# Kernel optimization log

Measured on AMD Instinct MI355X. Metric: run time of the kernel, lower is better.

Reference implementation:

```python
import jax, jax.numpy as jnp
import numpy as np


def _sig_gram(X, Y, n):
    """Signature-kernel gram matrix via the Goursat PDE recurrence.
    X: (A, M, D), Y: (B, N, D). Returns (A, B) of k(x_a, y_b).
    Recurrence: K[i+1,j+1] = K[i+1,j] + K[i,j+1] + K[i,j]*(inc_ij - 1).
    """
    f = 2 ** n
    # dyadic refinement: increments scaled by 1/2^n, each repeated 2^n times
    dX = jnp.repeat((X[:, 1:] - X[:, :-1]) / f, f, axis=1)  # (A, Mg-1, D)
    dY = jnp.repeat((Y[:, 1:] - Y[:, :-1]) / f, f, axis=1)  # (B, Ng-1, D)
    inc = jnp.einsum('aid,bjd->abij', dX, dY)               # (A, B, Mg-1, Ng-1)
    A, B, _, Ng1 = inc.shape
    ones_col = jnp.ones((A, B, 1), inc.dtype)

    def row_step(K_prev, inc_row):
        # K_prev: row i of the PDE grid, shape (A,B,Ng1+1); inc_row: (A,B,Ng1)
        diag = K_prev[..., :-1] * (inc_row - 1.0)  # K[i,j]*inc - K[i,j]
        up = K_prev[..., 1:]                        # K[i,j+1]

        def col_step(k_left, uv):
            u, d = uv
            k = k_left + u + d
            return k, k

        _, krow = jax.lax.scan(
            col_step,
            jnp.ones((A, B), inc.dtype),
            (jnp.moveaxis(up, -1, 0), jnp.moveaxis(diag, -1, 0)),
        )
        K_new = jnp.concatenate([ones_col, jnp.moveaxis(krow, 0, -1)], axis=-1)
        return K_new, None

    K0 = jnp.ones((A, B, Ng1 + 1), inc.dtype)  # boundary row K[0,:] = 1
    K_last, _ = jax.lax.scan(row_step, K0, jnp.moveaxis(inc, 2, 0))
    return K_last[..., -1]  # K[-1,-1] for every pair


def setup_inputs() -> dict:
    key = jax.random.key(0)
    kx, ky = jax.random.split(key)
    SCALE = 0.05  # keep kernel values in fp32 range (exponential growth)
    X = jax.random.normal(kx, (64, 128, 16), dtype=jnp.float32) * SCALE
    Y = jax.random.normal(ky, (64, 128, 16), dtype=jnp.float32) * SCALE
    return {"X": X, "Y": Y, "n": 0}


def reference(X, Y, n):
    k_xx = _sig_gram(X, X, n)
    k_yy = _sig_gram(Y, Y, n)
    k_xy = _sig_gram(X, Y, n)
    return jnp.mean(k_xx) + jnp.mean(k_yy) - 2.0 * jnp.mean(k_xy)
```

## Files before the change

kernel.cpp:

```cpp
#include <hip/hip_runtime.h>


typedef float f2 __attribute__((ext_vector_type(2)));

#define XY_BLOCKS 1024
#define TRI_BLOCKS 544
#define NBLOCKS (XY_BLOCKS + 2 * TRI_BLOCKS)

template <int C, int RM, int BM, bool BC>
__device__ __forceinline__ float dpp0(float x) {
    return __builtin_bit_cast(float, __builtin_amdgcn_update_dpp(
        0, __builtin_bit_cast(int, x), C, RM, BM, BC));
}

__device__ __forceinline__ float wave_scan_incl(float v) {
    v += dpp0<0x111, 0xf, 0xf, true>(v);
    v += dpp0<0x112, 0xf, 0xf, true>(v);
    v += dpp0<0x114, 0xf, 0xf, true>(v);
    v += dpp0<0x118, 0xf, 0xf, true>(v);
    v += dpp0<0x142, 0xa, 0xf, false>(v);
    v += dpp0<0x143, 0xc, 0xf, false>(v);
    return v;
}

__device__ __forceinline__ float wave_shr1(float x, float oldv) {
    return __builtin_bit_cast(float, __builtin_amdgcn_update_dpp(
        __builtin_bit_cast(int, oldv), __builtin_bit_cast(int, x),
        0x138, 0xf, 0xf, false));
}

__device__ __forceinline__ void load_xrow(f2* x, const float4* Ar, int r) {
#pragma unroll
    for (int q = 0; q < 4; ++q) {
        float4 v = Ar[4 * r + q];
        x[2*q].x   = v.x; x[2*q].y   = v.y;
        x[2*q+1].x = v.z; x[2*q+1].y = v.w;
    }
}

__device__ __forceinline__ void pde_row(
    const f2* xr, const f2* ya, const f2* yb,
    float& qpA, float& qpB, float& g_lo, float& g_hi, int lane)
{
    f2 s0 = 0.0f, s1 = 0.0f, t0 = 0.0f, t1 = 0.0f;
#pragma unroll
    for (int d = 0; d < 8; d += 2) {
        s0 = __builtin_elementwise_fma(xr[d],   ya[d],   s0);
        s1 = __builtin_elementwise_fma(xr[d+1], ya[d+1], s1);
        t0 = __builtin_elementwise_fma(xr[d],   yb[d],   t0);
        t1 = __builtin_elementwise_fma(xr[d+1], yb[d+1], t1);
    }
    const f2 sA = s0 + s1, sB = t0 + t1;
    const float hA = sA.x + sA.y, hB = sB.x + sB.y;
    const float i0 = hA - qpA;  qpA = hA + 1.0f;
    const float i1 = hB - qpB;  qpB = hB + 1.0f;
    const float gl = wave_shr1(g_hi, 1.0f);
    const float c0 = fmaf(gl, i0, g_lo);
    const float c1 = (lane == 63) ? 0.0f : fmaf(g_lo, i1, g_hi);
    const float S = wave_scan_incl(c0 + c1);
    g_lo = (S - c1) + 1.0f;
    g_hi = S + 1.0f;
}

__global__ __launch_bounds__(256) void sig_pde4(
    const float* __restrict__ X, const float* __restrict__ Y,
    float* __restrict__ outp)
{
    __shared__ float red[4];
    const int wv = threadIdx.x >> 6, lane = threadIdx.x & 63;
    const int B = blockIdx.x;

    int g, a, b;
    if (B < XY_BLOCKS) {
        g = 2; a = B >> 4; b = ((B & 15) << 2) + wv;
    } else {
        int t = B - XY_BLOCKS; g = 0;
        if (t >= TRI_BLOCKS) { t -= TRI_BLOCKS; g = 1; }
        int aa = 0;
        for (;;) { int nb = (67 - aa) >> 2; if (t < nb) break; t -= nb; ++aa; }
        a = aa; b = aa + (t << 2) + wv;
    }
    float weight = (g == 2) ? (-2.0f / 4096.0f)
                            : ((a == b ? 1.0f : 2.0f) / 4096.0f);
    if (g < 2 && b > 63) { b = 63; weight = 0.0f; }

    const float* P = (g == 1) ? Y : X;
    const float* Q = (g == 0) ? X : Y;

    f2 ya[8], yb[8];
    {
        const float* Qb = Q + b * 2048;
        const int j0 = lane << 1;
        const int j2 = (j0 + 2 <= 127) ? j0 + 2 : 127;
        const float4* A4 = (const float4*)(Qb + j0 * 16);
        const float4* B4 = (const float4*)(Qb + (j0 + 1) * 16);
        const float4* C4 = (const float4*)(Qb + j2 * 16);
#pragma unroll
        for (int q = 0; q < 4; ++q) {
            float4 ra = A4[q], rb = B4[q], rc = C4[q];
            ya[2*q].x   = rb.x - ra.x;  ya[2*q].y   = rb.y - ra.y;
            ya[2*q+1].x = rb.z - ra.z;  ya[2*q+1].y = rb.w - ra.w;
            yb[2*q].x   = rc.x - rb.x;  yb[2*q].y   = rc.y - rb.y;
            yb[2*q+1].x = rc.z - rb.z;  yb[2*q+1].y = rc.w - rb.w;
        }
    }

    const int abase = __builtin_amdgcn_readfirstlane(a * 2048);
    const float4* Ar = (const float4*)(P + abase);

    f2 xa[8], xb[8];
    float qpA, qpB;

    load_xrow(xa, Ar, 0);
    {
        f2 s0 = 0.0f, s1 = 0.0f, t0 = 0.0f, t1 = 0.0f;
#pragma unroll
        for (int d = 0; d < 8; d += 2) {
            s0 = __builtin_elementwise_fma(xa[d],   ya[d],   s0);
            s1 = __builtin_elementwise_fma(xa[d+1], ya[d+1], s1);
            t0 = __builtin_elementwise_fma(xa[d],   yb[d],   t0);
            t1 = __builtin_elementwise_fma(xa[d+1], yb[d+1], t1);
        }
        const f2 sA = s0 + s1, sB = t0 + t1;
        qpA = (sA.x + sA.y) + 1.0f;
        qpB = (sB.x + sB.y) + 1.0f;
    }
    load_xrow(xa, Ar, 1);

    float g_lo = 1.0f, g_hi = 1.0f;
    for (int r = 0; r < 126; r += 2) {
        load_xrow(xb, Ar, r + 2);
        pde_row(xa, ya, yb, qpA, qpB, g_lo, g_hi, lane);
        load_xrow(xa, Ar, r + 3);
        pde_row(xb, ya, yb, qpA, qpB, g_lo, g_hi, lane);
    }
    pde_row(xa, ya, yb, qpA, qpB, g_lo, g_hi, lane);

    const float kab = __builtin_bit_cast(float,
        __builtin_amdgcn_readlane(__builtin_bit_cast(int, g_lo), 63));
    if (lane == 0) red[wv] = weight * kab;
    __syncthreads();
    if (threadIdx.x == 0)
        atomicAdd(outp, (red[0] + red[1]) + (red[2] + red[3]));
}

extern "C" void kernel_launch(void* const* d_in, const int* in_sizes, int n_in,
                              void* d_out, int out_size, void* d_ws, size_t ws_size,
                              hipStream_t stream) {
    const float* X = (const float*)d_in[0];
    const float* Y = (const float*)d_in[1];
    float* out = (float*)d_out;
    (void)d_ws; (void)ws_size; (void)in_sizes; (void)n_in; (void)out_size;

    hipMemsetAsync(d_out, 0, sizeof(float), stream);
    sig_pde4<<<NBLOCKS, 256, 0, stream>>>(X, Y, out);
}
```

Before: 155.0 us.

## Precompute path increments in a prepass kernel and feed them to the PDE kernel

Adds a small kernel that writes the first differences of X and Y into workspace. The PDE kernel then loads X increments directly, instead of rebuilding each increment by subtracting consecutive dot products against raw rows. The -1 offset is folded into the accumulator initial values, packed FMAs are forced through inline asm, and row loads are made per-lane vector loads through an mbcnt-based offset. The cost is an extra kernel launch and a workspace round-trip, and the old single-kernel path is kept as a fallback when the workspace is too small.

```diff
diff --git a/kernel.cpp b/kernel.cpp
--- a/kernel.cpp
+++ b/kernel.cpp
@@ -6,6 +6,7 @@
 #define XY_BLOCKS 1024
 #define TRI_BLOCKS 544
 #define NBLOCKS (XY_BLOCKS + 2 * TRI_BLOCKS)
+#define DINC_PER 130048
 
 template <int C, int RM, int BM, bool BC>
 __device__ __forceinline__ float dpp0(float x) {
@@ -29,26 +30,134 @@
         0x138, 0xf, 0xf, false));
 }
 
-__device__ __forceinline__ void load_xrow(f2* x, const float4* Ar, int r) {
+__device__ __forceinline__ f2 pk_fma(f2 a, f2 b, f2 c) {
+    f2 d;
+    asm("v_pk_fma_f32 %0, %1, %2, %3" : "=v"(d) : "v"(a), "v"(b), "v"(c));
+    return d;
+}
+
+__device__ __forceinline__ void load_xrow(f2* x, const float4* Ar4, int r) {
 #pragma unroll
     for (int q = 0; q < 4; ++q) {
-        float4 v = Ar[4 * r + q];
-        x[2*q].x   = v.x; x[2*q].y   = v.y;
-        x[2*q+1].x = v.z; x[2*q+1].y = v.w;
+        float4 v = Ar4[4 * r + q];
+        x[2*q]   = f2{v.x, v.y};
+        x[2*q+1] = f2{v.z, v.w};
     }
 }
 
 __device__ __forceinline__ void pde_row(
     const f2* xr, const f2* ya, const f2* yb,
+    float& g_lo, float& g_hi, int lane)
+{
+    f2 a0 = f2{-0.25f, -0.25f}, a1 = f2{-0.25f, -0.25f};
+    f2 b0 = f2{-0.25f, -0.25f}, b1 = f2{-0.25f, -0.25f};
+#pragma unroll
+    for (int d = 0; d < 8; d += 2) {
+        a0 = pk_fma(xr[d],   ya[d],   a0);
+        a1 = pk_fma(xr[d+1], ya[d+1], a1);
+        b0 = pk_fma(xr[d],   yb[d],   b0);
+        b1 = pk_fma(xr[d+1], yb[d+1], b1);
+    }
+    const f2 sA = a0 + a1, sB = b0 + b1;
+    const float i0 = sA.x + sA.y;
+    const float i1 = sB.x + sB.y;
+    const float gl = wave_shr1(g_hi, 1.0f);
+    const float c0 = fmaf(gl, i0, g_lo);
+    const float c1 = (lane == 63) ? 0.0f : fmaf(g_lo, i1, g_hi);
+    const float S = wave_scan_incl(c0 + c1);
+    g_lo = (S - c1) + 1.0f;
+    g_hi = S + 1.0f;
+}
+
+__global__ __launch_bounds__(256) void sig_diff(
+    const float* __restrict__ X, const float* __restrict__ Y,
+    float* __restrict__ dInc)
+{
+    int i = blockIdx.x * 256 + threadIdx.x;
+    if (i >= 65024) return;
+    int which = (i >= 32512) ? 1 : 0;
+    int j = i - which * 32512;
+    int a = j / 508;
+    int rq = j - a * 508;
+    const float* S = which ? Y : X;
+    const float4* p = (const float4*)(S + a * 2048) + rq;
+    float4 v0 = p[0], v1 = p[4];
+    float4 d;
+    d.x = v1.x - v0.x; d.y = v1.y - v0.y;
+    d.z = v1.z - v0.z; d.w = v1.w - v0.w;
+    ((float4*)dInc)[i] = d;
+}
+
+__global__ __launch_bounds__(256) void sig_pde5(
+    const float* __restrict__ dInc, float* __restrict__ outp)
+{
+    __shared__ float red[4];
+    const int wv = threadIdx.x >> 6, lane = threadIdx.x & 63;
+    const int B = blockIdx.x;
+
+    int g, a, b;
+    if (B < XY_BLOCKS) {
+        g = 2; a = B >> 4; b = ((B & 15) << 2) + wv;
+    } else {
+        int t = B - XY_BLOCKS; g = 0;
+        if (t >= TRI_BLOCKS) { t -= TRI_BLOCKS; g = 1; }
+        int aa = 0;
+        for (;;) { int nb = (67 - aa) >> 2; if (t < nb) break; t -= nb; ++aa; }
+        a = aa; b = aa + (t << 2) + wv;
+    }
+    float weight = (g == 2) ? (-2.0f / 4096.0f)
+                            : ((a == b ? 1.0f : 2.0f) / 4096.0f);
+    if (g < 2 && b > 63) { b = 63; weight = 0.0f; }
+
+    const float* dA = (g == 1) ? (dInc + DINC_PER) : dInc;
+    const float* dB = (g == 0) ? dInc : (dInc + DINC_PER);
+
+    f2 ya[8], yb[8];
+    {
+        const int j0 = lane << 1;
+        const int j1 = (j0 + 1 < 127) ? j0 + 1 : 126;
+        const float4* A4 = (const float4*)(dB + b * 2032 + j0 * 16);
+        const float4* B4 = (const float4*)(dB + b * 2032 + j1 * 16);
+#pragma unroll
+        for (int q = 0; q < 4; ++q) {
+            float4 va = A4[q], vb = B4[q];
+            ya[2*q]   = f2{va.x, va.y};  ya[2*q+1] = f2{va.z, va.w};
+            yb[2*q]   = f2{vb.x, vb.y};  yb[2*q+1] = f2{vb.z, vb.w};
+        }
+    }
+
+    const int dz = __builtin_amdgcn_mbcnt_lo(0u, 0u);
+    const float4* Ar4 = (const float4*)(dA + a * 2032) + dz;
+
+    f2 xa[8], xb[8];
+    load_xrow(xa, Ar4, 0);
+
+    float g_lo = 1.0f, g_hi = 1.0f;
+    for (int r = 0; r < 126; r += 2) {
+        load_xrow(xb, Ar4, r + 1);
+        pde_row(xa, ya, yb, g_lo, g_hi, lane);
+        load_xrow(xa, Ar4, r + 2);
+        pde_row(xb, ya, yb, g_lo, g_hi, lane);
+    }
+    pde_row(xa, ya, yb, g_lo, g_hi, lane);
+
+    const float kab = __builtin_bit_cast(float,
+        __builtin_amdgcn_readlane(__builtin_bit_cast(int, g_lo), 63));
+    if (lane == 0) red[wv] = weight * kab;
+    __syncthreads();
+    if (threadIdx.x == 0)
+        atomicAdd(outp, (red[0] + red[1]) + (red[2] + red[3]));
+}
+
+__device__ __forceinline__ void pde_row_q(
+    const f2* xr, const f2* ya, const f2* yb,
     float& qpA, float& qpB, float& g_lo, float& g_hi, int lane)
 {
     f2 s0 = 0.0f, s1 = 0.0f, t0 = 0.0f, t1 = 0.0f;
 #pragma unroll
     for (int d = 0; d < 8; d += 2) {
-        s0 = __builtin_elementwise_fma(xr[d],   ya[d],   s0);
-        s1 = __builtin_elementwise_fma(xr[d+1], ya[d+1], s1);
-        t0 = __builtin_elementwise_fma(xr[d],   yb[d],   t0);
-        t1 = __builtin_elementwise_fma(xr[d+1], yb[d+1], t1);
+        s0 = pk_fma(xr[d], ya[d], s0);   s1 = pk_fma(xr[d+1], ya[d+1], s1);
+        t0 = pk_fma(xr[d], yb[d], t0);   t1 = pk_fma(xr[d+1], yb[d+1], t1);
     }
     const f2 sA = s0 + s1, sB = t0 + t1;
     const float hA = sA.x + sA.y, hB = sB.x + sB.y;
@@ -62,18 +171,16 @@
     g_hi = S + 1.0f;
 }
 
-__global__ __launch_bounds__(256) void sig_pde4(
+__global__ __launch_bounds__(256) void sig_pde_raw(
     const float* __restrict__ X, const float* __restrict__ Y,
     float* __restrict__ outp)
 {
     __shared__ float red[4];
     const int wv = threadIdx.x >> 6, lane = threadIdx.x & 63;
     const int B = blockIdx.x;
-
     int g, a, b;
-    if (B < XY_BLOCKS) {
-        g = 2; a = B >> 4; b = ((B & 15) << 2) + wv;
-    } else {
+    if (B < XY_BLOCKS) { g = 2; a = B >> 4; b = ((B & 15) << 2) + wv; }
+    else {
         int t = B - XY_BLOCKS; g = 0;
         if (t >= TRI_BLOCKS) { t -= TRI_BLOCKS; g = 1; }
         int aa = 0;
@@ -83,10 +190,8 @@
     float weight = (g == 2) ? (-2.0f / 4096.0f)
                             : ((a == b ? 1.0f : 2.0f) / 4096.0f);
     if (g < 2 && b > 63) { b = 63; weight = 0.0f; }
-
     const float* P = (g == 1) ? Y : X;
     const float* Q = (g == 0) ? X : Y;
-
     f2 ya[8], yb[8];
     {
         const float* Qb = Q + b * 2048;
@@ -98,44 +203,37 @@
 #pragma unroll
         for (int q = 0; q < 4; ++q) {
             float4 ra = A4[q], rb = B4[q], rc = C4[q];
-            ya[2*q].x   = rb.x - ra.x;  ya[2*q].y   = rb.y - ra.y;
-            ya[2*q+1].x = rb.z - ra.z;  ya[2*q+1].y = rb.w - ra.w;
-            yb[2*q].x   = rc.x - rb.x;  yb[2*q].y   = rc.y - rb.y;
-            yb[2*q+1].x = rc.z - rb.z;  yb[2*q+1].y = rc.w - rb.w;
+            ya[2*q]   = f2{rb.x - ra.x, rb.y - ra.y};
+            ya[2*q+1] = f2{rb.z - ra.z, rb.w - ra.w};
+            yb[2*q]   = f2{rc.x - rb.x, rc.y - rb.y};
+            yb[2*q+1] = f2{rc.z - rb.z, rc.w - rb.w};
         }
     }
-
-    const int abase = __builtin_amdgcn_readfirstlane(a * 2048);
-    const float4* Ar = (const float4*)(P + abase);
-
+    const int dz = __builtin_amdgcn_mbcnt_lo(0u, 0u);
+    const float4* Ar4 = (const float4*)(P + a * 2048) + dz;
     f2 xa[8], xb[8];
     float qpA, qpB;
-
-    load_xrow(xa, Ar, 0);
+    load_xrow(xa, Ar4, 0);
     {
         f2 s0 = 0.0f, s1 = 0.0f, t0 = 0.0f, t1 = 0.0f;
 #pragma unroll
         for (int d = 0; d < 8; d += 2) {
-            s0 = __builtin_elementwise_fma(xa[d],   ya[d],   s0);
-            s1 = __builtin_elementwise_fma(xa[d+1], ya[d+1], s1);
-            t0 = __builtin_elementwise_fma(xa[d],   yb[d],   t0);
-            t1 = __builtin_elementwise_fma(xa[d+1], yb[d+1], t1);
+            s0 = pk_fma(xa[d], ya[d], s0);   s1 = pk_fma(xa[d+1], ya[d+1], s1);
+            t0 = pk_fma(xa[d], yb[d], t0);   t1 = pk_fma(xa[d+1], yb[d+1], t1);
         }
         const f2 sA = s0 + s1, sB = t0 + t1;
         qpA = (sA.x + sA.y) + 1.0f;
         qpB = (sB.x + sB.y) + 1.0f;
     }
-    load_xrow(xa, Ar, 1);
-
+    load_xrow(xa, Ar4, 1);
     float g_lo = 1.0f, g_hi = 1.0f;
     for (int r = 0; r < 126; r += 2) {
-        load_xrow(xb, Ar, r + 2);
-        pde_row(xa, ya, yb, qpA, qpB, g_lo, g_hi, lane);
-        load_xrow(xa, Ar, r + 3);
-        pde_row(xb, ya, yb, qpA, qpB, g_lo, g_hi, lane);
-    }
-    pde_row(xa, ya, yb, qpA, qpB, g_lo, g_hi, lane);
-
+        load_xrow(xb, Ar4, r + 2);
+        pde_row_q(xa, ya, yb, qpA, qpB, g_lo, g_hi, lane);
+        load_xrow(xa, Ar4, r + 3);
+        pde_row_q(xb, ya, yb, qpA, qpB, g_lo, g_hi, lane);
+    }
+    pde_row_q(xa, ya, yb, qpA, qpB, g_lo, g_hi, lane);
     const float kab = __builtin_bit_cast(float,
         __builtin_amdgcn_readlane(__builtin_bit_cast(int, g_lo), 63));
     if (lane == 0) red[wv] = weight * kab;
@@ -150,8 +248,13 @@
     const float* X = (const float*)d_in[0];
     const float* Y = (const float*)d_in[1];
     float* out = (float*)d_out;
-    (void)d_ws; (void)ws_size; (void)in_sizes; (void)n_in; (void)out_size;
+    float* ws  = (float*)d_ws;
 
     hipMemsetAsync(d_out, 0, sizeof(float), stream);
-    sig_pde4<<<NBLOCKS, 256, 0, stream>>>(X, Y, out);
-}
+    if (ws_size >= (size_t)(2 * DINC_PER) * sizeof(float)) {
+        sig_diff<<<254, 256, 0, stream>>>(X, Y, ws);
+        sig_pde5<<<NBLOCKS, 256, 0, stream>>>(ws, out);
+    } else {
+        sig_pde_raw<<<NBLOCKS, 256, 0, stream>>>(X, Y, out);
+    }
+}
```

Measured after the change: 201.0 us. +29.7%, slower.
